# Kernel optimization log

Hardware: AMD Instinct MI355X
Metric: run time of the kernel (lower is better)

Reference implementation:

```python
import jax, jax.numpy as jnp
import numpy as np

ATTN = 128

def _gelu(x):
    return jax.nn.gelu(x, approximate=False)

def _mlp3(x, W1, b1, W2, b2, W3, b3):
    h = _gelu(x @ W1.T + b1)
    h = _gelu(h @ W2.T + b2)
    return h @ W3.T + b3

def setup_inputs() -> dict:
    key = jax.random.key(0)
    ks = jax.random.split(key, 32)
    B, K, M, C = 128, 64, 2048, 32
    QD, AD, H = 128, 128, 256
    s = 0.02
    d = {}
    d['g'] = jax.random.normal(ks[0], (B, K, 3), dtype=jnp.float32)
    d['query'] = jax.random.normal(ks[1], (M, QD), dtype=jnp.float32) * s
    d['qW'] = jax.random.normal(ks[2], (AD, QD), dtype=jnp.float32) * s
    d['qb'] = jnp.zeros((AD,), jnp.float32)
    d['kW'] = jax.random.normal(ks[3], (AD, 1), dtype=jnp.float32) * s
    d['kb'] = jnp.zeros((AD,), jnp.float32)
    # global_mlp: K -> H -> H -> H
    d['gm_W1'] = jax.random.normal(ks[4], (H, K), dtype=jnp.float32) * s
    d['gm_b1'] = jnp.zeros((H,), jnp.float32)
    d['gm_W2'] = jax.random.normal(ks[5], (H, H), dtype=jnp.float32) * s
    d['gm_b2'] = jnp.zeros((H,), jnp.float32)
    d['gm_W3'] = jax.random.normal(ks[6], (H, H), dtype=jnp.float32) * s
    d['gm_b3'] = jnp.zeros((H,), jnp.float32)
    # point_mlp: (H+QD+1) -> H -> H -> H
    d['pm_W1'] = jax.random.normal(ks[7], (H, H + QD + 1), dtype=jnp.float32) * s
    d['pm_b1'] = jnp.zeros((H,), jnp.float32)
    d['pm_W2'] = jax.random.normal(ks[8], (H, H), dtype=jnp.float32) * s
    d['pm_b2'] = jnp.zeros((H,), jnp.float32)
    d['pm_W3'] = jax.random.normal(ks[9], (H, H), dtype=jnp.float32) * s
    d['pm_b3'] = jnp.zeros((H,), jnp.float32)
    d['tW'] = jax.random.normal(ks[10], (C, H), dtype=jnp.float32) * s
    d['tb'] = jnp.zeros((C,), jnp.float32)
    d['wW'] = jax.random.normal(ks[11], (1, H), dtype=jnp.float32) * s
    d['wb'] = jnp.zeros((1,), jnp.float32)
    d['cW'] = jax.random.normal(ks[12], (1, H), dtype=jnp.float32) * s
    d['cb'] = jnp.zeros((1,), jnp.float32)
    return d

def reference(g, query, qW, qb, kW, kb,
              gm_W1, gm_b1, gm_W2, gm_b2, gm_W3, gm_b3,
              pm_W1, pm_b1, pm_W2, pm_b2, pm_W3, pm_b3,
              tW, tb, wW, wb, cW, cb):
    B, K, _ = g.shape
    M = query.shape[0]
    inv = jnp.linalg.norm(g, axis=-1)                    # (B,K)
    Q = query @ qW.T + qb                                # (M,AD)
    Kk = inv[..., None] * kW[:, 0] + kb                  # (B,K,AD) Linear(1->AD)
    scores = jnp.einsum('md,bkd->bmk', Q, Kk) / jnp.sqrt(jnp.float32(Q.shape[-1]))
    A = jax.nn.softmax(scores, axis=-1)                  # (B,M,K)
    y = jnp.einsum('bmk,bkd->bmd', A, g)                 # (B,M,3)
    global_s = _mlp3(inv, gm_W1, gm_b1, gm_W2, gm_b2, gm_W3, gm_b3)  # (B,H)
    attended_inv = jnp.einsum('bmk,bk->bm', A, inv)      # (B,M)
    s_in = jnp.concatenate([
        jnp.broadcast_to(global_s[:, None, :], (B, M, global_s.shape[-1])),
        jnp.broadcast_to(query[None], (B, M, query.shape[-1])),
        attended_inv[..., None],
    ], axis=-1)                                          # (B,M,H+QD+1)
    s = _mlp3(s_in, pm_W1, pm_b1, pm_W2, pm_b2, pm_W3, pm_b3)  # (B,M,H)
    type_logits = s @ tW.T + tb                          # (B,M,C)
    weight_logits = (s @ wW.T + wb)[..., 0]              # (B,M)
    gate = jnp.clip(jax.nn.sigmoid(s @ cW.T + cb), 0.0, 1.0)  # (B,M,1)
    y = y * gate
    return (y, type_logits, weight_logits)
```

## Files before the change

### kernel.cpp

```cpp
#include <hip/hip_runtime.h>
#include <math.h>


typedef __attribute__((ext_vector_type(8))) short short8;
typedef __attribute__((ext_vector_type(4))) float f32x4;

__device__ __forceinline__ unsigned short bf16_rne(float f){
    union { float f; unsigned u; } v; v.f = f;
    return (unsigned short)((v.u + 0x7FFFu + ((v.u >> 16) & 1u)) >> 16);
}

__device__ __forceinline__ float gelu_f(float x){
    float z  = x * 0.70710678118654752f;
    float az = fabsf(z);
    float t  = __builtin_amdgcn_rcpf(1.0f + 0.3275911f * az);
    float p  = t*(0.254829592f + t*(-0.284496736f + t*(1.421413741f + t*(-1.453152027f + t*1.061405429f))));
    float e  = __expf(-az*az);
    float er = copysignf(1.0f - p*e, z);
    return 0.5f * x * (1.0f + er);
}

__device__ __forceinline__ float gelu_fast(float x){
    float x2 = x*x;
    float p  = fmaf(x2, -0.1029433f, -2.3022082f);
    float u  = x*p;
    float e  = __builtin_amdgcn_exp2f(u);
    float r  = __builtin_amdgcn_rcpf(1.0f + e);
    return x*r;
}

__global__ void k_pre1(const float* __restrict__ g, const float* __restrict__ qW,
                       const float* __restrict__ qb, const float* __restrict__ kW,
                       const float* __restrict__ query, const float* __restrict__ pmW1,
                       const float* __restrict__ pmW2, const float* __restrict__ pmW3,
                       const float* __restrict__ pmb3,
                       const float* __restrict__ gmW1, const float* __restrict__ gmW2,
                       const float* __restrict__ gmW3,
                       const float* __restrict__ tW, const float* __restrict__ tb,
                       const float* __restrict__ wW, const float* __restrict__ wb,
                       const float* __restrict__ cW, const float* __restrict__ cb,
                       float* __restrict__ invg, float* __restrict__ vg, float* __restrict__ s0g,
                       unsigned short* __restrict__ w2b, unsigned short* __restrict__ wheadb,
                       float* __restrict__ bheadg,
                       unsigned short* __restrict__ w1qb, unsigned short* __restrict__ queryb,
                       float* __restrict__ gmW1t, float* __restrict__ gmW2t,
                       float* __restrict__ gmW3t, float* __restrict__ w1gt,
                       float* __restrict__ w385g) {
    const int bid = blockIdx.x, tid = threadIdx.x;
    if (bid < 32) {
        int idx = bid*256 + tid;
        const float* p = g + idx*3;
        invg[idx] = sqrtf(p[0]*p[0] + p[1]*p[1] + p[2]*p[2]);
    } else if (bid == 32) {
        if (tid < 128) {
            float acc = 0.f;
            for (int d = 0; d < 128; ++d) acc += qW[d*128 + tid] * kW[d];
            vg[tid] = acc;
            if (tid == 0) {
                float s = 0.f;
                for (int d = 0; d < 128; ++d) s += qb[d] * kW[d];
                *s0g = s;
            }
        }
    } else if (bid < 97) {
        int o = (bid - 33)*1024 + tid*4;
        float4 x = *(const float4*)&pmW2[o];
        union { unsigned short u[4]; uint2 v; } r;
        r.u[0] = bf16_rne(x.x); r.u[1] = bf16_rne(x.y);
        r.u[2] = bf16_rne(x.z); r.u[3] = bf16_rne(x.w);
        *(uint2*)&w2b[o] = r.v;
    } else if (bid < 131) {
        __shared__ float hw[256];
        int c = bid - 97;
        const float* src = (c < 32) ? (tW + c*256) : ((c == 32) ? wW : cW);
        hw[tid] = src[tid];
        __syncthreads();
        float acc = 0.f;
        for (int j = 0; j < 256; ++j) acc += hw[j] * pmW3[j*256 + tid];
        wheadb[c*256 + tid] = bf16_rne(acc);
        if (tid == 0) {
            float bacc = (c < 32) ? tb[c] : ((c == 32) ? wb[0] : cb[0]);
            for (int j = 0; j < 256; ++j) bacc += hw[j] * pmb3[j];
            bheadg[c] = bacc;
        }
    } else if (bid < 163) {
        int o = (bid - 131)*1024 + tid*4;
        int n = o >> 7, k = o & 127;
        union { unsigned short u[4]; uint2 v; } r;
        #pragma unroll
        for (int i = 0; i < 4; ++i) r.u[i] = bf16_rne(pmW1[n*385 + 256 + k + i]);
        *(uint2*)&w1qb[o] = r.v;
    } else if (bid < 227) {
        int base = (bid - 163)*4096 + tid*4;
        #pragma unroll
        for (int it = 0; it < 4; ++it) {
            int o = base + it*1024;
            float4 x = *(const float4*)&query[o];
            union { unsigned short u[4]; uint2 v; } r;
            r.u[0] = bf16_rne(x.x); r.u[1] = bf16_rne(x.y);
            r.u[2] = bf16_rne(x.z); r.u[3] = bf16_rne(x.w);
            *(uint2*)&queryb[o] = r.v;
        }
    } else if (bid < 291) {
        int o = (bid - 227)*1024 + tid*4;
        int i = o >> 8, j = o & 255;
        float4 r = { gmW2[j*256+i], gmW2[(j+1)*256+i], gmW2[(j+2)*256+i], gmW2[(j+3)*256+i] };
        *(float4*)&gmW2t[o] = r;
    } else if (bid < 355) {
        int o = (bid - 291)*1024 + tid*4;
        int i = o >> 8, j = o & 255;
        float4 r = { gmW3[j*256+i], gmW3[(j+1)*256+i], gmW3[(j+2)*256+i], gmW3[(j+3)*256+i] };
        *(float4*)&gmW3t[o] = r;
    } else if (bid < 419) {
        int o = (bid - 355)*1024 + tid*4;
        int i = o >> 8, j = o & 255;
        float4 r = { pmW1[j*385+i], pmW1[(j+1)*385+i], pmW1[(j+2)*385+i], pmW1[(j+3)*385+i] };
        *(float4*)&w1gt[o] = r;
    } else if (bid < 435) {
        int o = (bid - 419)*1024 + tid*4;
        int k = o >> 8, j = o & 255;
        float4 r = { gmW1[j*64+k], gmW1[(j+1)*64+k], gmW1[(j+2)*64+k], gmW1[(j+3)*64+k] };
        *(float4*)&gmW1t[o] = r;
    } else {
        w385g[tid] = pmW1[tid*385 + 384];
    }
}

__global__ void k_pre2(const float* __restrict__ query, const float* __restrict__ vg,
                       const float* __restrict__ s0g, const float* __restrict__ invg,
                       const float* __restrict__ gmW1t, const float* __restrict__ gmb1,
                       const float* __restrict__ gmW2t, const float* __restrict__ gmb2,
                       const float* __restrict__ gmW3t, const float* __restrict__ gmb3,
                       const float* __restrict__ w1gt, const float* __restrict__ pmb1,
                       float* __restrict__ ag, float* __restrict__ u1g) {
    const int bid = blockIdx.x, tid = threadIdx.x;
    if (bid < 8) {
        __shared__ float vs[128];
        if (tid < 128) vs[tid] = vg[tid];
        __syncthreads();
        int m = bid*256 + tid;
        const float4* qp = (const float4*)(query + m*128);
        float acc = *s0g;
        #pragma unroll 8
        for (int e4 = 0; e4 < 32; ++e4) {
            float4 q = qp[e4];
            acc += q.x*vs[e4*4] + q.y*vs[e4*4+1] + q.z*vs[e4*4+2] + q.w*vs[e4*4+3];
        }
        ag[m] = acc * 0.08838834764831845f;
    } else {
        __shared__ float s_in[64];
        __shared__ float s_h[256];
        __shared__ float s_h2[256];
        int b = bid - 8;
        if (tid < 64) s_in[tid] = invg[b*64 + tid];
        __syncthreads();
        float acc = gmb1[tid];
        #pragma unroll 8
        for (int k = 0; k < 64; ++k) acc += gmW1t[k*256 + tid] * s_in[k];
        s_h[tid] = gelu_f(acc);
        __syncthreads();
        acc = gmb2[tid];
        #pragma unroll 8
        for (int i = 0; i < 256; ++i) acc += gmW2t[i*256 + tid] * s_h[i];
        s_h2[tid] = gelu_f(acc);
        __syncthreads();
        acc = gmb3[tid];
        #pragma unroll 8
        for (int i = 0; i < 256; ++i) acc += gmW3t[i*256 + tid] * s_h2[i];
        __syncthreads();
        s_h[tid] = acc;
        __syncthreads();
        float u = pmb1[tid];
        #pragma unroll 8
        for (int i = 0; i < 256; ++i) u += w1gt[i*256 + tid] * s_h[i];
        u1g[b*256 + tid] = u;
    }
}

__global__ __launch_bounds__(256, 4)
void k_main(const float* __restrict__ g,
            const float* __restrict__ invg, const float* __restrict__ ag,
            const float* __restrict__ u1g, const float* __restrict__ w385g,
            const float* __restrict__ pmb2,
            const unsigned short* __restrict__ queryb, const unsigned short* __restrict__ w1qb,
            const unsigned short* __restrict__ w2b, const unsigned short* __restrict__ wheadb,
            const float* __restrict__ bheadg, float* __restrict__ out) {
    __shared__ __align__(16) unsigned short hb[64*264];
    __shared__ float invs[64], gsl[192], u1s[256], w385s[256], pmb2s[256];
    __shared__ float ainv_s[64], y0s[192];

    const int tid = threadIdx.x;
    const int bid = blockIdx.x;
    const int b  = bid >> 5;
    const int m0 = (bid & 31) << 6;

    if (tid < 64)  invs[tid] = invg[b*64 + tid];
    if (tid < 192) gsl[tid]  = g[b*192 + tid];
    u1s[tid]   = u1g[b*256 + tid];
    w385s[tid] = w385g[tid];
    pmb2s[tid] = pmb2[tid];
    __syncthreads();

    {
        const int r = tid >> 2, sub = tid & 3;
        const float am = ag[m0 + r];
        const int kb = sub * 16;
        float mx = -1e30f;
        #pragma unroll
        for (int i = 0; i < 16; ++i) mx = fmaxf(mx, invs[kb + i] * am);
        #pragma unroll
        for (int d = 1; d < 4; d <<= 1) mx = fmaxf(mx, __shfl_xor(mx, d, 64));
        float den = 0.f, ai = 0.f, y0 = 0.f, y1 = 0.f, y2 = 0.f;
        #pragma unroll
        for (int i = 0; i < 16; ++i) {
            const int k = kb + i;
            const float iv = invs[k];
            const float e = __expf(iv * am - mx);
            den += e; ai += e * iv;
            y0 += e * gsl[k*3+0]; y1 += e * gsl[k*3+1]; y2 += e * gsl[k*3+2];
        }
        #pragma unroll
        for (int d = 1; d < 4; d <<= 1) {
            den += __shfl_xor(den, d, 64);
            ai  += __shfl_xor(ai , d, 64);
            y0  += __shfl_xor(y0 , d, 64);
            y1  += __shfl_xor(y1 , d, 64);
            y2  += __shfl_xor(y2 , d, 64);
        }
        if (sub == 0) {
            const float id = 1.0f / den;
            ainv_s[r] = ai * id;
            y0s[r*3+0] = y0*id; y0s[r*3+1] = y1*id; y0s[r*3+2] = y2*id;
        }
    }
    __syncthreads();

    const int w = tid >> 6, lane = tid & 63;
    const int q = lane >> 4, ln = lane & 15;

    {
        f32x4 acc[4][4];
        #pragma unroll
        for (int mt = 0; mt < 4; ++mt)
            #pragma unroll
            for (int nt = 0; nt < 4; ++nt) acc[mt][nt] = (f32x4){0.f,0.f,0.f,0.f};
        #pragma unroll
        for (int kk = 0; kk < 4; ++kk) {
            const int kc = kk*32 + q*8;
            short8 afr[4], bfr[4];
            #pragma unroll
            for (int mt = 0; mt < 4; ++mt)
                afr[mt] = *(const short8*)&queryb[(m0 + mt*16 + ln)*128 + kc];
            #pragma unroll
            for (int nt = 0; nt < 4; ++nt)
                bfr[nt] = *(const short8*)&w1qb[(w*64 + nt*16 + ln)*128 + kc];
            #pragma unroll
            for (int mt = 0; mt < 4; ++mt)
                #pragma unroll
                for (int nt = 0; nt < 4; ++nt)
                    acc[mt][nt] = __builtin_amdgcn_mfma_f32_16x16x32_bf16(afr[mt], bfr[nt], acc[mt][nt], 0, 0, 0);
        }
        #pragma unroll
        for (int mt = 0; mt < 4; ++mt) {
            #pragma unroll
            for (int nt = 0; nt < 4; ++nt) {
                const int n = w*64 + nt*16 + ln;
                const float u1v = u1s[n], wv = w385s[n];
                #pragma unroll
                for (int rg = 0; rg < 4; ++rg) {
                    const int r = mt*16 + q*4 + rg;
                    const float x = acc[mt][nt][rg] + u1v + ainv_s[r]*wv;
                    hb[r*264 + n] = bf16_rne(gelu_fast(x));
                }
            }
        }
    }
    __syncthreads();

    f32x4 acc[4][4];
    #pragma unroll
    for (int mt = 0; mt < 4; ++mt)
        #pragma unroll
        for (int nt = 0; nt < 4; ++nt) acc[mt][nt] = (f32x4){0.f,0.f,0.f,0.f};

    #pragma unroll 2
    for (int kk = 0; kk < 8; ++kk) {
        const int kc = kk*32 + q*8;
        short8 afrag[4], bfrag[4];
        #pragma unroll
        for (int mt = 0; mt < 4; ++mt)
            afrag[mt] = *(const short8*)&hb[(mt*16 + ln)*264 + kc];
        #pragma unroll
        for (int nt = 0; nt < 4; ++nt)
            bfrag[nt] = *(const short8*)&w2b[(w*64 + nt*16 + ln)*256 + kc];
        #pragma unroll
        for (int mt = 0; mt < 4; ++mt)
            #pragma unroll
            for (int nt = 0; nt < 4; ++nt)
                acc[mt][nt] = __builtin_amdgcn_mfma_f32_16x16x32_bf16(afrag[mt], bfrag[nt], acc[mt][nt], 0, 0, 0);
    }
    __syncthreads();

    #pragma unroll
    for (int mt = 0; mt < 4; ++mt) {
        #pragma unroll
        for (int nt = 0; nt < 4; ++nt) {
            const int n = w*64 + nt*16 + ln;
            const float bb = pmb2s[n];
            #pragma unroll
            for (int rg = 0; rg < 4; ++rg) {
                const int r = mt*16 + q*4 + rg;
                hb[r*264 + n] = bf16_rne(gelu_fast(acc[mt][nt][rg] + bb));
            }
        }
    }
    __syncthreads();

    f32x4 accA0 = {0.f,0.f,0.f,0.f}, accA1 = {0.f,0.f,0.f,0.f}, accB = {0.f,0.f,0.f,0.f};
    const int rr = w*16 + ln;
    const int cb2 = (ln < 2) ? (32 + ln) : 33;
    #pragma unroll 2
    for (int kk = 0; kk < 8; ++kk) {
        const int kc = kk*32 + q*8;
        short8 bh = *(const short8*)&hb[rr*264 + kc];
        short8 a0 = *(const short8*)&wheadb[ ln      *256 + kc];
        short8 a1 = *(const short8*)&wheadb[(16 + ln)*256 + kc];
        short8 a2 = *(const short8*)&wheadb[ cb2     *256 + kc];
        accA0 = __builtin_amdgcn_mfma_f32_16x16x32_bf16(a0, bh, accA0, 0, 0, 0);
        accA1 = __builtin_amdgcn_mfma_f32_16x16x32_bf16(a1, bh, accA1, 0, 0, 0);
        accB  = __builtin_amdgcn_mfma_f32_16x16x32_bf16(a2, bh, accB , 0, 0, 0);
    }
    {
        const size_t row = (size_t)b*2048 + m0 + rr;
        const int c0 = q*4;
        f32x4 r0 = accA0 + *(const f32x4*)&bheadg[c0];
        f32x4 r1 = accA1 + *(const f32x4*)&bheadg[16 + c0];
        *(f32x4*)&out[786432 + row*32 + c0]      = r0;
        *(f32x4*)&out[786432 + row*32 + 16 + c0] = r1;
        if (q == 0) {
            out[9175040 + row] = accB[0] + bheadg[32];
            float gv = accB[1] + bheadg[33];
            float gt = 1.0f / (1.0f + __expf(-gv));
            gt = fminf(fmaxf(gt, 0.0f), 1.0f);
            float* yo = out + row*3;
            yo[0] = y0s[rr*3+0] * gt;
            yo[1] = y0s[rr*3+1] * gt;
            yo[2] = y0s[rr*3+2] * gt;
        }
    }
}

extern "C" void kernel_launch(void* const* d_in, const int* in_sizes, int n_in,
                              void* d_out, int out_size, void* d_ws, size_t ws_size,
                              hipStream_t stream) {
    const float* g     = (const float*)d_in[0];
    const float* query = (const float*)d_in[1];
    const float* qW    = (const float*)d_in[2];
    const float* qb    = (const float*)d_in[3];
    const float* kW    = (const float*)d_in[4];
    const float* gmW1  = (const float*)d_in[6];
    const float* gmb1  = (const float*)d_in[7];
    const float* gmW2  = (const float*)d_in[8];
    const float* gmb2  = (const float*)d_in[9];
    const float* gmW3  = (const float*)d_in[10];
    const float* gmb3  = (const float*)d_in[11];
    const float* pmW1  = (const float*)d_in[12];
    const float* pmb1  = (const float*)d_in[13];
    const float* pmW2  = (const float*)d_in[14];
    const float* pmb2  = (const float*)d_in[15];
    const float* pmW3  = (const float*)d_in[16];
    const float* pmb3  = (const float*)d_in[17];
    const float* tW    = (const float*)d_in[18];
    const float* tb    = (const float*)d_in[19];
    const float* wW    = (const float*)d_in[20];
    const float* wb    = (const float*)d_in[21];
    const float* cW    = (const float*)d_in[22];
    const float* cb    = (const float*)d_in[23];
    float* out = (float*)d_out;

    float* ws    = (float*)d_ws;
    float* invg  = ws;
    float* ag    = ws + 8192;
    float* vg    = ws + 10240;
    float* s0g   = ws + 10368;
    float* u1g   = ws + 10496;
    float* gmW1t = ws + 43264;
    float* gmW2t = ws + 59648;
    float* gmW3t = ws + 125184;
    float* w1gt  = ws + 190720;
    float* w385g = ws + 256256;
    float* bheadg= ws + 256512;
    unsigned short* w2b    = (unsigned short*)(ws + 256576);
    unsigned short* wheadb = (unsigned short*)(ws + 289344);
    unsigned short* w1qb   = (unsigned short*)(ws + 293696);
    unsigned short* queryb = (unsigned short*)(ws + 310080);

    hipLaunchKernelGGL(k_pre1, dim3(436), dim3(256), 0, stream,
                       g, qW, qb, kW, query, pmW1, pmW2, pmW3, pmb3,
                       gmW1, gmW2, gmW3,
                       tW, tb, wW, wb, cW, cb,
                       invg, vg, s0g, w2b, wheadb, bheadg,
                       w1qb, queryb, gmW1t, gmW2t, gmW3t, w1gt, w385g);
    hipLaunchKernelGGL(k_pre2, dim3(136), dim3(256), 0, stream,
                       query, vg, s0g, invg,
                       gmW1t, gmb1, gmW2t, gmb2, gmW3t, gmb3, w1gt, pmb1,
                       ag, u1g);
    hipLaunchKernelGGL(k_main, dim3(4096), dim3(256), 0, stream,
                       g, invg, ag, u1g, w385g, pmb2,
                       queryb, w1qb, w2b, wheadb, bheadg, out);
}
```

Measured before the change: 316.2 us.

## Hoist batch-invariant query projection GEMM out of main kernel into precompute

The query·W1q product does not depend on the batch index, yet it was recomputed by every one of the 4096 main blocks. It is now computed once per 64-row tile in k_pre2 (32 extra blocks), stored as fp32 u2g, and loaded in k_main with vectorized reads before the GELU, then packed to bf16. The W2 and head-weight fragments are also software-prefetched one k-step ahead, and bf16 packing uses the paired conversion intrinsic. In exchange, each block now reads 64 KB of fp32 from global/L2 instead of doing 64 MFMAs, and register pressure rises from the prefetch buffers.

```diff
diff --git a/kernel.cpp b/kernel.cpp
--- a/kernel.cpp
+++ b/kernel.cpp
@@ -1,4 +1,5 @@
 #include <hip/hip_runtime.h>
+#include <hip/hip_bf16.h>
 #include <math.h>
 
 
@@ -8,6 +9,12 @@
 __device__ __forceinline__ unsigned short bf16_rne(float f){
     union { float f; unsigned u; } v; v.f = f;
     return (unsigned short)((v.u + 0x7FFFu + ((v.u >> 16) & 1u)) >> 16);
+}
+__device__ __forceinline__ unsigned pk_bf16(float a, float b){
+    float2 t; t.x = a; t.y = b;
+    __hip_bfloat162 h = __float22bfloat162_rn(t);
+    union { __hip_bfloat162 h; unsigned u; } cv; cv.h = h;
+    return cv.u;
 }
 
 __device__ __forceinline__ float gelu_f(float x){
@@ -132,7 +139,10 @@
                        const float* __restrict__ gmW2t, const float* __restrict__ gmb2,
                        const float* __restrict__ gmW3t, const float* __restrict__ gmb3,
                        const float* __restrict__ w1gt, const float* __restrict__ pmb1,
-                       float* __restrict__ ag, float* __restrict__ u1g) {
+                       const unsigned short* __restrict__ queryb,
+                       const unsigned short* __restrict__ w1qb,
+                       float* __restrict__ ag, float* __restrict__ u1g,
+                       float* __restrict__ u2g) {
     const int bid = blockIdx.x, tid = threadIdx.x;
     if (bid < 8) {
         __shared__ float vs[128];
@@ -147,7 +157,7 @@
             acc += q.x*vs[e4*4] + q.y*vs[e4*4+1] + q.z*vs[e4*4+2] + q.w*vs[e4*4+3];
         }
         ag[m] = acc * 0.08838834764831845f;
-    } else {
+    } else if (bid < 136) {
         __shared__ float s_in[64];
         __shared__ float s_h[256];
         __shared__ float s_h2[256];
@@ -174,20 +184,53 @@
         #pragma unroll 8
         for (int i = 0; i < 256; ++i) u += w1gt[i*256 + tid] * s_h[i];
         u1g[b*256 + tid] = u;
+    } else {
+        const int m0 = (bid - 136)*64;
+        const int w = tid >> 6, lane = tid & 63;
+        const int q = lane >> 4, ln = lane & 15;
+        f32x4 acc[4][4];
+        #pragma unroll
+        for (int mt = 0; mt < 4; ++mt)
+            #pragma unroll
+            for (int nt = 0; nt < 4; ++nt) acc[mt][nt] = (f32x4){0.f,0.f,0.f,0.f};
+        #pragma unroll
+        for (int kk = 0; kk < 4; ++kk) {
+            const int kc = kk*32 + q*8;
+            short8 afr[4], bfr[4];
+            #pragma unroll
+            for (int mt = 0; mt < 4; ++mt)
+                afr[mt] = *(const short8*)&queryb[(m0 + mt*16 + ln)*128 + kc];
+            #pragma unroll
+            for (int nt = 0; nt < 4; ++nt)
+                bfr[nt] = *(const short8*)&w1qb[(w*64 + nt*16 + ln)*128 + kc];
+            #pragma unroll
+            for (int mt = 0; mt < 4; ++mt)
+                #pragma unroll
+                for (int nt = 0; nt < 4; ++nt)
+                    acc[mt][nt] = __builtin_amdgcn_mfma_f32_16x16x32_bf16(afr[mt], bfr[nt], acc[mt][nt], 0, 0, 0);
+        }
+        #pragma unroll
+        for (int mt = 0; mt < 4; ++mt)
+            #pragma unroll
+            for (int nt = 0; nt < 4; ++nt) {
+                const int n = w*64 + nt*16 + ln;
+                #pragma unroll
+                for (int rg = 0; rg < 4; ++rg)
+                    u2g[(size_t)(m0 + mt*16 + q*4 + rg)*256 + n] = acc[mt][nt][rg];
+            }
     }
 }
 
 __global__ __launch_bounds__(256, 4)
 void k_main(const float* __restrict__ g,
             const float* __restrict__ invg, const float* __restrict__ ag,
-            const float* __restrict__ u1g, const float* __restrict__ w385g,
-            const float* __restrict__ pmb2,
-            const unsigned short* __restrict__ queryb, const unsigned short* __restrict__ w1qb,
+            const float* __restrict__ u1g, const float* __restrict__ u2g,
+            const float* __restrict__ w385g, const float* __restrict__ pmb2,
             const unsigned short* __restrict__ w2b, const unsigned short* __restrict__ wheadb,
             const float* __restrict__ bheadg, float* __restrict__ out) {
     __shared__ __align__(16) unsigned short hb[64*264];
-    __shared__ float invs[64], gsl[192], u1s[256], w385s[256], pmb2s[256];
-    __shared__ float ainv_s[64], y0s[192];
+    __shared__ __align__(16) float u1s[256], w385s[256], pmb2s[256];
+    __shared__ float invs[64], gsl[192], ainv_s[64], y0s[192];
 
     const int tid = threadIdx.x;
     const int bid = blockIdx.x;
@@ -235,69 +278,64 @@
     }
     __syncthreads();
 
+    {
+        const int ln16 = tid & 15, rbase = tid >> 4;
+        #pragma unroll
+        for (int rr = 0; rr < 4; ++rr) {
+            const int r = rr*16 + rbase;
+            const float aiv = ainv_s[r];
+            const float* u2p = u2g + (size_t)(m0 + r)*256;
+            #pragma unroll
+            for (int k = 0; k < 4; ++k) {
+                const int c = ln16*4 + k*64;
+                float4 x  = *(const float4*)&u2p[c];
+                float4 uv = *(const float4*)&u1s[c];
+                float4 wv = *(const float4*)&w385s[c];
+                float g0 = gelu_fast(x.x + uv.x + aiv*wv.x);
+                float g1 = gelu_fast(x.y + uv.y + aiv*wv.y);
+                float g2 = gelu_fast(x.z + uv.z + aiv*wv.z);
+                float g3 = gelu_fast(x.w + uv.w + aiv*wv.w);
+                uint2 pk; pk.x = pk_bf16(g0, g1); pk.y = pk_bf16(g2, g3);
+                *(uint2*)&hb[r*264 + c] = pk;
+            }
+        }
+    }
+    __syncthreads();
+
     const int w = tid >> 6, lane = tid & 63;
     const int q = lane >> 4, ln = lane & 15;
 
+    f32x4 acc[4][4];
+    #pragma unroll
+    for (int mt = 0; mt < 4; ++mt)
+        #pragma unroll
+        for (int nt = 0; nt < 4; ++nt) acc[mt][nt] = (f32x4){0.f,0.f,0.f,0.f};
+
     {
-        f32x4 acc[4][4];
-        #pragma unroll
-        for (int mt = 0; mt < 4; ++mt)
-            #pragma unroll
-            for (int nt = 0; nt < 4; ++nt) acc[mt][nt] = (f32x4){0.f,0.f,0.f,0.f};
-        #pragma unroll
-        for (int kk = 0; kk < 4; ++kk) {
+        const unsigned short* w2p = w2b + (w*64 + ln)*256 + q*8;
+        short8 bcur[4], bnxt[4];
+        #pragma unroll
+        for (int nt = 0; nt < 4; ++nt) bcur[nt] = *(const short8*)(w2p + nt*4096);
+        #pragma unroll
+        for (int kk = 0; kk < 8; ++kk) {
+            if (kk < 7) {
+                #pragma unroll
+                for (int nt = 0; nt < 4; ++nt)
+                    bnxt[nt] = *(const short8*)(w2p + nt*4096 + (kk+1)*32);
+            }
+            short8 afrag[4];
             const int kc = kk*32 + q*8;
-            short8 afr[4], bfr[4];
             #pragma unroll
             for (int mt = 0; mt < 4; ++mt)
-                afr[mt] = *(const short8*)&queryb[(m0 + mt*16 + ln)*128 + kc];
-            #pragma unroll
-            for (int nt = 0; nt < 4; ++nt)
-                bfr[nt] = *(const short8*)&w1qb[(w*64 + nt*16 + ln)*128 + kc];
+                afrag[mt] = *(const short8*)&hb[(mt*16 + ln)*264 + kc];
             #pragma unroll
             for (int mt = 0; mt < 4; ++mt)
                 #pragma unroll
                 for (int nt = 0; nt < 4; ++nt)
-                    acc[mt][nt] = __builtin_amdgcn_mfma_f32_16x16x32_bf16(afr[mt], bfr[nt], acc[mt][nt], 0, 0, 0);
-        }
-        #pragma unroll
-        for (int mt = 0; mt < 4; ++mt) {
-            #pragma unroll
-            for (int nt = 0; nt < 4; ++nt) {
-                const int n = w*64 + nt*16 + ln;
-                const float u1v = u1s[n], wv = w385s[n];
-                #pragma unroll
-                for (int rg = 0; rg < 4; ++rg) {
-                    const int r = mt*16 + q*4 + rg;
-                    const float x = acc[mt][nt][rg] + u1v + ainv_s[r]*wv;
-                    hb[r*264 + n] = bf16_rne(gelu_fast(x));
-                }
-            }
-        }
-    }
-    __syncthreads();
-
-    f32x4 acc[4][4];
-    #pragma unroll
-    for (int mt = 0; mt < 4; ++mt)
-        #pragma unroll
-        for (int nt = 0; nt < 4; ++nt) acc[mt][nt] = (f32x4){0.f,0.f,0.f,0.f};
-
-    #pragma unroll 2
-    for (int kk = 0; kk < 8; ++kk) {
-        const int kc = kk*32 + q*8;
-        short8 afrag[4], bfrag[4];
-        #pragma unroll
-        for (int mt = 0; mt < 4; ++mt)
-            afrag[mt] = *(const short8*)&hb[(mt*16 + ln)*264 + kc];
-        #pragma unroll
-        for (int nt = 0; nt < 4; ++nt)
-            bfrag[nt] = *(const short8*)&w2b[(w*64 + nt*16 + ln)*256 + kc];
-        #pragma unroll
-        for (int mt = 0; mt < 4; ++mt)
-            #pragma unroll
-            for (int nt = 0; nt < 4; ++nt)
-                acc[mt][nt] = __builtin_amdgcn_mfma_f32_16x16x32_bf16(afrag[mt], bfrag[nt], acc[mt][nt], 0, 0, 0);
+                    acc[mt][nt] = __builtin_amdgcn_mfma_f32_16x16x32_bf16(afrag[mt], bcur[nt], acc[mt][nt], 0, 0, 0);
+            #pragma unroll
+            for (int nt = 0; nt < 4; ++nt) bcur[nt] = bnxt[nt];
+        }
     }
     __syncthreads();
 
@@ -307,28 +345,42 @@
         for (int nt = 0; nt < 4; ++nt) {
             const int n = w*64 + nt*16 + ln;
             const float bb = pmb2s[n];
-            #pragma unroll
-            for (int rg = 0; rg < 4; ++rg) {
-                const int r = mt*16 + q*4 + rg;
-                hb[r*264 + n] = bf16_rne(gelu_fast(acc[mt][nt][rg] + bb));
-            }
-        }
-    }
+            const int r0 = mt*16 + q*4;
+            float h0 = gelu_fast(acc[mt][nt][0] + bb);
+            float h1 = gelu_fast(acc[mt][nt][1] + bb);
+            float h2 = gelu_fast(acc[mt][nt][2] + bb);
+            float h3 = gelu_fast(acc[mt][nt][3] + bb);
+            unsigned p01 = pk_bf16(h0, h1);
+            unsigned p23 = pk_bf16(h2, h3);
+            hb[(r0+0)*264 + n] = (unsigned short)(p01 & 0xFFFF);
+            hb[(r0+1)*264 + n] = (unsigned short)(p01 >> 16);
+            hb[(r0+2)*264 + n] = (unsigned short)(p23 & 0xFFFF);
+            hb[(r0+3)*264 + n] = (unsigned short)(p23 >> 16);
+        }
+    }
+
+    const int cb2 = (ln < 2) ? (32 + ln) : 33;
+    const unsigned short* whp = wheadb + q*8;
+    short8 wf0 = *(const short8*)(whp +  ln      *256);
+    short8 wf1 = *(const short8*)(whp + (16 + ln)*256);
+    short8 wf2 = *(const short8*)(whp +  cb2     *256);
     __syncthreads();
 
     f32x4 accA0 = {0.f,0.f,0.f,0.f}, accA1 = {0.f,0.f,0.f,0.f}, accB = {0.f,0.f,0.f,0.f};
     const int rr = w*16 + ln;
-    const int cb2 = (ln < 2) ? (32 + ln) : 33;
-    #pragma unroll 2
+    #pragma unroll
     for (int kk = 0; kk < 8; ++kk) {
-        const int kc = kk*32 + q*8;
-        short8 bh = *(const short8*)&hb[rr*264 + kc];
-        short8 a0 = *(const short8*)&wheadb[ ln      *256 + kc];
-        short8 a1 = *(const short8*)&wheadb[(16 + ln)*256 + kc];
-        short8 a2 = *(const short8*)&wheadb[ cb2     *256 + kc];
-        accA0 = __builtin_amdgcn_mfma_f32_16x16x32_bf16(a0, bh, accA0, 0, 0, 0);
-        accA1 = __builtin_amdgcn_mfma_f32_16x16x32_bf16(a1, bh, accA1, 0, 0, 0);
-        accB  = __builtin_amdgcn_mfma_f32_16x16x32_bf16(a2, bh, accB , 0, 0, 0);
+        short8 wn0, wn1, wn2;
+        if (kk < 7) {
+            wn0 = *(const short8*)(whp +  ln      *256 + (kk+1)*32);
+            wn1 = *(const short8*)(whp + (16 + ln)*256 + (kk+1)*32);
+            wn2 = *(const short8*)(whp +  cb2     *256 + (kk+1)*32);
+        }
+        short8 bh = *(const short8*)&hb[rr*264 + kk*32 + q*8];
+        accA0 = __builtin_amdgcn_mfma_f32_16x16x32_bf16(wf0, bh, accA0, 0, 0, 0);
+        accA1 = __builtin_amdgcn_mfma_f32_16x16x32_bf16(wf1, bh, accA1, 0, 0, 0);
+        accB  = __builtin_amdgcn_mfma_f32_16x16x32_bf16(wf2, bh, accB , 0, 0, 0);
+        wf0 = wn0; wf1 = wn1; wf2 = wn2;
     }
     {
         const size_t row = (size_t)b*2048 + m0 + rr;
@@ -394,6 +446,7 @@
     unsigned short* wheadb = (unsigned short*)(ws + 289344);
     unsigned short* w1qb   = (unsigned short*)(ws + 293696);
     unsigned short* queryb = (unsigned short*)(ws + 310080);
+    float* u2g   = ws + 441152;
 
     hipLaunchKernelGGL(k_pre1, dim3(436), dim3(256), 0, stream,
                        g, qW, qb, kW, query, pmW1, pmW2, pmW3, pmb3,
@@ -401,11 +454,12 @@
                        tW, tb, wW, wb, cW, cb,
                        invg, vg, s0g, w2b, wheadb, bheadg,
                        w1qb, queryb, gmW1t, gmW2t, gmW3t, w1gt, w385g);
-    hipLaunchKernelGGL(k_pre2, dim3(136), dim3(256), 0, stream,
+    hipLaunchKernelGGL(k_pre2, dim3(168), dim3(256), 0, stream,
                        query, vg, s0g, invg,
                        gmW1t, gmb1, gmW2t, gmb2, gmW3t, gmb3, w1gt, pmb1,
-                       ag, u1g);
+                       queryb, w1qb,
+                       ag, u1g, u2g);
     hipLaunchKernelGGL(k_main, dim3(4096), dim3(256), 0, stream,
-                       g, invg, ag, u1g, w385g, pmb2,
-                       queryb, w1qb, w2b, wheadb, bheadg, out);
-}
+                       g, invg, ag, u1g, u2g, w385g, pmb2,
+                       w2b, wheadb, bheadg, out);
+}
```

Measured after the change: 269.6 us. 1.17x faster.
